# Optimization experiments

Measured on AMD Instinct MI355X. Metric: run time of the kernel, lower is better.

The kernel has to match this reference:

```python
import jax, jax.numpy as jnp
import numpy as np

MEMORY_SIZE = 32768
DIM_K = 256
DIM_V = 256
B = 2048
OLD_SIZE = 16384


def setup_inputs() -> dict:
    key = jax.random.key(0)
    k1, k2, k3, k4, k5 = jax.random.split(key, 5)
    return {
        "q": jax.random.normal(k1, (B, DIM_K), dtype=jnp.float32),
        "k": jax.random.normal(k2, (B, DIM_K), dtype=jnp.float32),
        "v": jax.random.normal(k3, (B, DIM_V), dtype=jnp.float32),
        "K_cache": jax.random.normal(k4, (MEMORY_SIZE, DIM_K), dtype=jnp.float32),
        "V_cache": jax.random.normal(k5, (MEMORY_SIZE, DIM_V), dtype=jnp.float32),
        "old_size": OLD_SIZE,
    }


def reference(q, k, v, K_cache, V_cache, old_size):
    b, dim_k = q.shape
    new_size = old_size + b  # static python int
    # write the new chunk of keys/values into the cache
    K = jax.lax.dynamic_update_slice(K_cache, k, (old_size, 0))
    V = jax.lax.dynamic_update_slice(V_cache, v, (old_size, 0))
    Kv = K[:new_size]  # [new_size, dim_k]
    Vv = V[:new_size]  # [new_size, dim_v]
    # scaled dot-product scores: [b, new_size]
    scores = (q @ Kv.T) * (1.0 / (dim_k ** 0.5))
    # causal mask: query i (global pos old_size+i) may attend keys j <= old_size+i
    key_idx = jnp.arange(new_size)[None, :]
    query_idx = jnp.arange(old_size, new_size)[:, None]
    scores = jnp.where(key_idx > query_idx, -jnp.inf, scores)
    p = jax.nn.softmax(scores, axis=-1)
    return p @ Vv  # [b, dim_v]
```

## Files before the change

### kernel.cpp

```cpp
#include <hip/hip_runtime.h>
#include <hip/hip_bf16.h>
#include <cstdint>

typedef __attribute__((ext_vector_type(8)))  short s8b;
typedef __attribute__((ext_vector_type(4)))  short s4b;
typedef __attribute__((ext_vector_type(16))) float f16v;
typedef __attribute__((ext_vector_type(4)))  unsigned u4v;

#define MFMA32(a,b,c) __builtin_amdgcn_mfma_f32_32x32x16_bf16((a),(b),(c),0,0,0)

#define OLDN   16384
#define NEWB   2048
#define DHEAD  256
#define NTOTAL 18432
#define NTILES 576
#define EXPSC  0.09016844005556021f

static __device__ __forceinline__ short f2bf(float f) {
    unsigned u = __float_as_uint(f);
    unsigned r = (u + 0x7fffu + ((u >> 16) & 1u)) >> 16;
    return (short)r;
}
static __device__ __forceinline__ int slot_key(int s) {
    return (s & 3) + 8 * ((s >> 2) & 1) + 4 * ((s >> 3) & 1) + 16 * (s >> 4);
}

__global__ void cvt_kernel(const float* __restrict__ Kc, const float* __restrict__ kn,
                           const float* __restrict__ Vc, const float* __restrict__ vn,
                           s8b* __restrict__ Ksw, s8b* __restrict__ Vsw) {
    const int t   = blockIdx.x;
    const int tid = threadIdx.x;
    if (blockIdx.y == 0) {
#pragma unroll
        for (int i = 0; i < 4; ++i) {
            int chunk = tid + 256 * i;
            int l = chunk & 63;
            int b = chunk >> 6;
            int row = 32 * t + (l & 31);
            int col = 16 * b + 8 * (l >> 5);
            const float* src = (row < OLDN) ? Kc + (size_t)row * DHEAD + col
                                            : kn + (size_t)(row - OLDN) * DHEAD + col;
            float4 f0 = *(const float4*)src;
            float4 f1 = *(const float4*)(src + 4);
            s8b o;
            o[0]=f2bf(f0.x); o[1]=f2bf(f0.y); o[2]=f2bf(f0.z); o[3]=f2bf(f0.w);
            o[4]=f2bf(f1.x); o[5]=f2bf(f1.y); o[6]=f2bf(f1.z); o[7]=f2bf(f1.w);
            Ksw[(size_t)t * 1024 + chunk] = o;
        }
    } else {
#pragma unroll
        for (int i = 0; i < 4; ++i) {
            int chunk = tid + 256 * i;
            int l = chunk & 63;
            int b = chunk >> 6;
            int m = 32 * (b >> 1) + (l & 31);
            int sbase = 16 * (b & 1) + 8 * (l >> 5);
            s8b o;
#pragma unroll
            for (int j = 0; j < 8; ++j) {
                int row = 32 * t + slot_key(sbase + j);
                float v = (row < OLDN) ? Vc[(size_t)row * DHEAD + m]
                                       : vn[(size_t)(row - OLDN) * DHEAD + m];
                o[j] = f2bf(v);
            }
            Vsw[(size_t)t * 1024 + chunk] = o;
        }
    }
}

__global__ __launch_bounds__(256, 2)
void attn_kernel(const float* __restrict__ q,
                 const s8b* __restrict__ Ksw, const s8b* __restrict__ Vsw,
                 short* __restrict__ OPb, float* __restrict__ L, int SPLIT) {
    __shared__ short V_lds[16 * 512];

    const int bx   = blockIdx.x;
    const int s    = bx % SPLIT;
    const int qb   = bx / SPLIT;
    const int q0   = qb * 128;
    const int tid  = threadIdx.x;
    const int w    = tid >> 6;
    const int lane = tid & 63;
    const int lc   = lane & 31;
    const int h    = lane >> 5;

    s8b qf[16];
    {
        const int qrow = q0 + 32 * w + lc;
        const float* qp = q + (size_t)qrow * DHEAD + 8 * h;
#pragma unroll
        for (int c = 0; c < 16; ++c) {
            float4 f0 = *(const float4*)(qp + 16 * c);
            float4 f1 = *(const float4*)(qp + 16 * c + 4);
            s8b o;
            o[0]=f2bf(f0.x*EXPSC); o[1]=f2bf(f0.y*EXPSC); o[2]=f2bf(f0.z*EXPSC); o[3]=f2bf(f0.w*EXPSC);
            o[4]=f2bf(f1.x*EXPSC); o[5]=f2bf(f1.y*EXPSC); o[6]=f2bf(f1.z*EXPSC); o[7]=f2bf(f1.w*EXPSC);
            qf[c] = o;
        }
    }

    f16v acc[8];
#pragma unroll
    for (int c = 0; c < 8; ++c)
#pragma unroll
        for (int r = 0; r < 16; ++r) acc[c][r] = 0.f;
    float lsum = 0.f;

    const int nt_total = (OLDN + q0 + 128) >> 5;
    const int tb  = nt_total / SPLIT;
    const int rem = nt_total % SPLIT;
    const int t0  = s * tb + (s < rem ? s : rem);
    const int tcnt = tb + (s < rem ? 1 : 0);
    const int qbase = OLDN + q0 + 32 * w;

    const s8b* kp = Ksw + (size_t)t0 * 1024 + lane;
    const s8b* vp = Vsw + (size_t)t0 * 1024 + (size_t)(4 * w) * 64 + lane;
    short* vlds_w = &V_lds[(4 * w) * 512 + lane * 8];
    const short* vlds_r = &V_lds[lane * 8];

    for (int t = t0; t < t0 + tcnt; ++t, kp += 1024, vp += 1024) {
        const int kk = t << 5;

        s8b vstage[4];
#pragma unroll
        for (int i = 0; i < 4; ++i) vstage[i] = vp[i * 64];

        f16v sacc0, sacc1;
#pragma unroll
        for (int r = 0; r < 16; ++r) { sacc0[r] = 0.f; sacc1[r] = 0.f; }
#pragma unroll
        for (int c = 0; c < 8; ++c) {
            s8b k0 = kp[(2 * c) * 64];
            s8b k1 = kp[(2 * c + 1) * 64];
            sacc0 = MFMA32(k0, qf[2 * c],     sacc0);
            sacc1 = MFMA32(k1, qf[2 * c + 1], sacc1);
        }

        const bool domask = (kk + 31 > qbase);
        unsigned pk[8];
#pragma unroll
        for (int i = 0; i < 8; ++i) {
            const int r0 = 2 * i, r1 = 2 * i + 1;
            float ev0 = __builtin_exp2f(sacc0[r0] + sacc1[r0]);
            float ev1 = __builtin_exp2f(sacc0[r1] + sacc1[r1]);
            if (domask) {
                if (kk + (r0 & 3) + 8 * (r0 >> 2) + 4 * h > qbase + lc) ev0 = 0.f;
                if (kk + (r1 & 3) + 8 * (r1 >> 2) + 4 * h > qbase + lc) ev1 = 0.f;
            }
            lsum += ev0 + ev1;
            pk[i] = __builtin_amdgcn_perm(__float_as_uint(ev1), __float_as_uint(ev0), 0x07060302u);
        }
        s8b pf0 = __builtin_bit_cast(s8b, (u4v){pk[0], pk[1], pk[2], pk[3]});
        s8b pf1 = __builtin_bit_cast(s8b, (u4v){pk[4], pk[5], pk[6], pk[7]});

#pragma unroll
        for (int i = 0; i < 4; ++i) *(s8b*)(vlds_w + i * 512) = vstage[i];
        __syncthreads();

#pragma unroll
        for (int c = 0; c < 8; ++c) {
            s8b v0 = *(const s8b*)(vlds_r + (2 * c) * 512);
            s8b v1 = *(const s8b*)(vlds_r + (2 * c + 1) * 512);
            acc[c] = MFMA32(v0, pf0, acc[c]);
            acc[c] = MFMA32(v1, pf1, acc[c]);
        }
        __syncthreads();
    }

    lsum += __shfl_xor(lsum, 32);

    const int qrow = q0 + 32 * w + lc;
    const size_t sbase = (size_t)s * NEWB;
    short* op_row = OPb + (sbase + qrow) * DHEAD;
#pragma unroll
    for (int c = 0; c < 8; ++c)
#pragma unroll
        for (int g = 0; g < 4; ++g) {
            s4b o4;
            o4[0] = f2bf(acc[c][4 * g]);
            o4[1] = f2bf(acc[c][4 * g + 1]);
            o4[2] = f2bf(acc[c][4 * g + 2]);
            o4[3] = f2bf(acc[c][4 * g + 3]);
            *(s4b*)(op_row + 32 * c + 8 * g + 4 * h) = o4;
        }
    if (h == 0) L[sbase + qrow] = lsum;
}

__global__ void combine_kernel(const short* __restrict__ OPb, const float* __restrict__ L,
                               float* __restrict__ out, int SPLIT) {
    const int row = blockIdx.x;
    const int col = threadIdx.x;
    float num = 0.f, den = 0.f;
    for (int s = 0; s < SPLIT; ++s) {
        size_t r = (size_t)s * NEWB + row;
        unsigned u = (unsigned)(unsigned short)OPb[r * DHEAD + col];
        num += __uint_as_float(u << 16);
        den += L[r];
    }
    out[(size_t)row * DHEAD + col] = num / den;
}

extern "C" void kernel_launch(void* const* d_in, const int* in_sizes, int n_in,
                              void* d_out, int out_size, void* d_ws, size_t ws_size,
                              hipStream_t stream) {
    const float* q  = (const float*)d_in[0];
    const float* kn = (const float*)d_in[1];
    const float* vn = (const float*)d_in[2];
    const float* Kc = (const float*)d_in[3];
    const float* Vc = (const float*)d_in[4];
    float* out = (float*)d_out;

    char* ws = (char*)d_ws;
    const size_t KB_BYTES = (size_t)NTOTAL * DHEAD * 2;
    s8b* Ksw = (s8b*)(ws);
    s8b* Vsw = (s8b*)(ws + KB_BYTES);
    const size_t PART_BASE = 2 * KB_BYTES;

    const size_t per_split = (size_t)NEWB * DHEAD * 2 + (size_t)NEWB * 4;
    size_t avail = (ws_size > PART_BASE) ? (ws_size - PART_BASE) : 0;
    int SPLIT = (int)(avail / per_split);
    if (SPLIT > 32) SPLIT = 32;
    if (SPLIT < 1)  SPLIT = 1;

    short* OPb = (short*)(ws + PART_BASE);
    float* L   = (float*)(ws + PART_BASE + (size_t)SPLIT * NEWB * DHEAD * 2);

    cvt_kernel<<<dim3(NTILES, 2), 256, 0, stream>>>(Kc, kn, Vc, vn, Ksw, Vsw);
    attn_kernel<<<16 * SPLIT, 256, 0, stream>>>(q, Ksw, Vsw, OPb, L, SPLIT);
    combine_kernel<<<NEWB, 256, 0, stream>>>(OPb, L, out, SPLIT);
}
```

Before: 187.2 us.

## Double-buffer K and V tiles in LDS with async global-to-LDS loads

```diff
diff --git a/kernel.cpp b/kernel.cpp
--- a/kernel.cpp
+++ b/kernel.cpp
@@ -23,6 +23,12 @@
 }
 static __device__ __forceinline__ int slot_key(int s) {
     return (s & 3) + 8 * ((s >> 2) & 1) + 4 * ((s >> 3) & 1) + 16 * (s >> 4);
+}
+
+static __device__ __forceinline__ void dma16(const void* g, void* l) {
+    __builtin_amdgcn_global_load_lds((const __attribute__((address_space(1))) unsigned int*)g,
+                                     (__attribute__((address_space(3))) unsigned int*)l,
+                                     16, 0, 0);
 }
 
 __global__ void cvt_kernel(const float* __restrict__ Kc, const float* __restrict__ kn,
@@ -72,7 +78,7 @@
 void attn_kernel(const float* __restrict__ q,
                  const s8b* __restrict__ Ksw, const s8b* __restrict__ Vsw,
                  short* __restrict__ OPb, float* __restrict__ L, int SPLIT) {
-    __shared__ short V_lds[16 * 512];
+    __shared__ short smem[2 * 16384];
 
     const int bx   = blockIdx.x;
     const int s    = bx % SPLIT;
@@ -111,27 +117,37 @@
     const int rem = nt_total % SPLIT;
     const int t0  = s * tb + (s < rem ? s : rem);
     const int tcnt = tb + (s < rem ? 1 : 0);
+    const int tend = t0 + tcnt;
     const int qbase = OLDN + q0 + 32 * w;
 
-    const s8b* kp = Ksw + (size_t)t0 * 1024 + lane;
-    const s8b* vp = Vsw + (size_t)t0 * 1024 + (size_t)(4 * w) * 64 + lane;
-    short* vlds_w = &V_lds[(4 * w) * 512 + lane * 8];
-    const short* vlds_r = &V_lds[lane * 8];
-
-    for (int t = t0; t < t0 + tcnt; ++t, kp += 1024, vp += 1024) {
+    const s8b* gseg = (w < 2) ? (Ksw + (size_t)(8 * w) * 64 + lane)
+                              : (Vsw + (size_t)(8 * (w - 2)) * 64 + lane);
+    short* lseg = &smem[(8 * w) * 512 + lane * 8];
+
+    {
+        const s8b* g0 = gseg + (size_t)t0 * 1024;
+#pragma unroll
+        for (int i = 0; i < 8; ++i) dma16(g0 + i * 64, lseg + i * 512);
+        const int t1 = (t0 + 1 < tend) ? t0 + 1 : t0;
+        const s8b* g1 = gseg + (size_t)t1 * 1024;
+#pragma unroll
+        for (int i = 0; i < 8; ++i) dma16(g1 + i * 64, lseg + 16384 + i * 512);
+    }
+    __syncthreads();
+
+    int cur = 0;
+    for (int t = t0; t < tend; ++t, cur ^= 1) {
         const int kk = t << 5;
-
-        s8b vstage[4];
-#pragma unroll
-        for (int i = 0; i < 4; ++i) vstage[i] = vp[i * 64];
+        const short* Kbuf = &smem[cur * 16384 + lane * 8];
+        const short* Vbuf = Kbuf + 8192;
 
         f16v sacc0, sacc1;
 #pragma unroll
         for (int r = 0; r < 16; ++r) { sacc0[r] = 0.f; sacc1[r] = 0.f; }
 #pragma unroll
         for (int c = 0; c < 8; ++c) {
-            s8b k0 = kp[(2 * c) * 64];
-            s8b k1 = kp[(2 * c + 1) * 64];
+            s8b k0 = *(const s8b*)(Kbuf + (2 * c) * 512);
+            s8b k1 = *(const s8b*)(Kbuf + (2 * c + 1) * 512);
             sacc0 = MFMA32(k0, qf[2 * c],     sacc0);
             sacc1 = MFMA32(k1, qf[2 * c + 1], sacc1);
         }
@@ -154,17 +170,22 @@
         s8b pf1 = __builtin_bit_cast(s8b, (u4v){pk[4], pk[5], pk[6], pk[7]});
 
 #pragma unroll
-        for (int i = 0; i < 4; ++i) *(s8b*)(vlds_w + i * 512) = vstage[i];
-        __syncthreads();
-
-#pragma unroll
         for (int c = 0; c < 8; ++c) {
-            s8b v0 = *(const s8b*)(vlds_r + (2 * c) * 512);
-            s8b v1 = *(const s8b*)(vlds_r + (2 * c + 1) * 512);
+            s8b v0 = *(const s8b*)(Vbuf + (2 * c) * 512);
+            s8b v1 = *(const s8b*)(Vbuf + (2 * c + 1) * 512);
             acc[c] = MFMA32(v0, pf0, acc[c]);
             acc[c] = MFMA32(v1, pf1, acc[c]);
         }
+
         __syncthreads();
+
+        {
+            const int tp = (t + 2 < tend) ? t + 2 : tend - 1;
+            const s8b* gp = gseg + (size_t)tp * 1024;
+            short* lp = lseg + cur * 16384;
+#pragma unroll
+            for (int i = 0; i < 8; ++i) dma16(gp + i * 64, lp + i * 512);
+        }
     }
 
     lsum += __shfl_xor(lsum, 32);
```

Result: faster. 168.6 us (-10.0%).
